# Optimization experiments

Measured on AMD Instinct MI355X. Metric: run time of the kernel, lower is better.

## Reference

```python
import jax, jax.numpy as jnp
import numpy as np

DIM = 1024
HEADS = 16
HEAD_DIM = DIM // HEADS
B, N = 2, 2048
SCALE = 1.0 / np.float32(np.sqrt(DIM))  # original scales by sqrt(dim), not sqrt(head_dim)


def setup_inputs() -> dict:
    key = jax.random.key(0)
    ks = jax.random.split(key, 9)
    s = 0.02
    return {
        "x": jax.random.normal(ks[0], (B, N, DIM), dtype=jnp.float32),
        "Wq": jax.random.normal(ks[1], (DIM, DIM), dtype=jnp.float32) * s,
        "bq": jax.random.normal(ks[2], (DIM,), dtype=jnp.float32) * s,
        "Wk": jax.random.normal(ks[3], (DIM, DIM), dtype=jnp.float32) * s,
        "bk": jax.random.normal(ks[4], (DIM,), dtype=jnp.float32) * s,
        "Wv": jax.random.normal(ks[5], (DIM, DIM), dtype=jnp.float32) * s,
        "bv": jax.random.normal(ks[6], (DIM,), dtype=jnp.float32) * s,
        "Wo": jax.random.normal(ks[7], (DIM, DIM), dtype=jnp.float32) * s,
        "bo": jax.random.normal(ks[8], (DIM,), dtype=jnp.float32) * s,
    }


def _split_heads(t):
    # torch.stack(torch.split(t, head_dim, -1), dim=0) -> (H, B, N, head_dim)
    b, n, _ = t.shape
    return jnp.moveaxis(t.reshape(b, n, HEADS, HEAD_DIM), 2, 0)


def reference(x, Wq, bq, Wk, bk, Wv, bv, Wo, bo):
    q = _split_heads(x @ Wq.T + bq)  # (H,B,N,d)
    k = _split_heads(x @ Wk.T + bk)
    v = _split_heads(x @ Wv.T + bv)
    # NOTE: original computes K @ Q^T (K rows attend over Q rows), scaled by sqrt(dim)
    scores = jnp.einsum("hbnd,hbmd->hbnm", k, q) * SCALE  # (H,B,N,N)
    attn = jax.nn.softmax(scores, axis=-1)
    out = jnp.einsum("hbnm,hbmd->hbnd", attn, v)  # (H,B,N,d)
    out = jnp.moveaxis(out, 0, 2).reshape(x.shape[0], x.shape[1], DIM)  # (B,N,H*d)
    return out @ Wo.T + bo
```

## Files before the change

kernel.cpp:

```cpp
#include <hip/hip_runtime.h>
#include <hip/hip_bf16.h>
#include <cstdint>
#include <cstddef>

typedef __bf16 bf16_t;
typedef __bf16 bf16x4 __attribute__((ext_vector_type(4)));
typedef __bf16 bf16x8 __attribute__((ext_vector_type(8)));
typedef float  f32x4  __attribute__((ext_vector_type(4)));
typedef float  f32x16 __attribute__((ext_vector_type(16)));
typedef unsigned int u32;
typedef unsigned int u32x4 __attribute__((ext_vector_type(4)));

#define DIM_   1024
#define HEADS_ 16
#define HD_    64
#define BB_    2
#define NN_    2048
#define MTOT   (BB_*NN_)
static constexpr float SCALE_ = 0.03125f;
static constexpr float EXPC_  = 0.045084220027780106f;

__device__ __forceinline__ float exp2_hw(float x) {
    float r;
    asm("v_exp_f32 %0, %1" : "=v"(r) : "v"(x));
    return r;
}

__global__ __launch_bounds__(256) void cvt_all(
    const float* __restrict__ X,
    const float* __restrict__ W0, const float* __restrict__ W1,
    const float* __restrict__ W2, const float* __restrict__ W3,
    bf16_t* __restrict__ xo,
    bf16_t* __restrict__ o0, bf16_t* __restrict__ o1,
    bf16_t* __restrict__ o2, bf16_t* __restrict__ o3)
{
    const int bid = blockIdx.x;
    const float* src;
    bf16_t* dst;
    int lb;
    if (bid < 2048) { src = X; dst = xo; lb = bid; }
    else {
        const int w = (bid - 2048) >> 9;
        lb = (bid - 2048) & 511;
        src = (w == 0) ? W0 : (w == 1) ? W1 : (w == 2) ? W2 : W3;
        dst = (w == 0) ? o0 : (w == 1) ? o1 : (w == 2) ? o2 : o3;
    }
    const size_t i = ((size_t)lb * 256 + threadIdx.x) * 8;
    f32x4 a = *(const f32x4*)(src + i);
    f32x4 b = *(const f32x4*)(src + i + 4);
    bf16x8 o;
    o[0] = (bf16_t)a.x; o[1] = (bf16_t)a.y; o[2] = (bf16_t)a.z; o[3] = (bf16_t)a.w;
    o[4] = (bf16_t)b.x; o[5] = (bf16_t)b.y; o[6] = (bf16_t)b.z; o[7] = (bf16_t)b.w;
    *(bf16x8*)(dst + i) = o;
}

__device__ __forceinline__ void gld16(const bf16_t* g, bf16_t* l) {
    __builtin_amdgcn_global_load_lds(
        (const __attribute__((address_space(1))) unsigned int*)g,
        (__attribute__((address_space(3))) unsigned int*)l, 16, 0, 0);
}

__global__ __launch_bounds__(512) void gemm_qkv(
    const bf16_t* __restrict__ A,
    const bf16_t* __restrict__ Wq, const bf16_t* __restrict__ Wk, const bf16_t* __restrict__ Wv,
    const float* __restrict__ bq, const float* __restrict__ bk, const float* __restrict__ bv,
    bf16_t* __restrict__ Cq, bf16_t* __restrict__ Ck, bf16_t* __restrict__ Cv)
{
    __shared__ __align__(16) bf16_t As[128 * 64];
    __shared__ __align__(16) bf16_t Bs[3][64 * 64];

    const int tid  = threadIdx.x;
    const int lane = tid & 63;
    const int w    = tid >> 6;
    const int wr   = w >> 1;
    const int wc   = w & 1;
    const int bn   = blockIdx.x;
    const int bm   = blockIdx.y;

    const int l15 = lane & 15;
    const int g   = lane >> 4;

    const int srow = lane >> 3;
    const int scol = (lane & 7) * 8;

    f32x4 aq[2][2], ak[2][2], av[2][2];
    #pragma unroll
    for (int i = 0; i < 2; i++)
        #pragma unroll
        for (int j = 0; j < 2; j++) {
            aq[i][j] = (f32x4){0.f, 0.f, 0.f, 0.f};
            ak[i][j] = (f32x4){0.f, 0.f, 0.f, 0.f};
            av[i][j] = (f32x4){0.f, 0.f, 0.f, 0.f};
        }

    for (int kb = 0; kb < DIM_; kb += 64) {
        __syncthreads();
        #pragma unroll
        for (int c2 = 0; c2 < 2; c2++) {
            const int chunk = w * 2 + c2;
            gld16(A + (size_t)(bm * 128 + chunk * 8 + srow) * DIM_ + kb + scol,
                  As + chunk * 512);
        }
        gld16(Wq + (size_t)(bn * 64 + w * 8 + srow) * DIM_ + kb + scol, &Bs[0][0] + w * 512);
        gld16(Wk + (size_t)(bn * 64 + w * 8 + srow) * DIM_ + kb + scol, &Bs[1][0] + w * 512);
        gld16(Wv + (size_t)(bn * 64 + w * 8 + srow) * DIM_ + kb + scol, &Bs[2][0] + w * 512);
        __syncthreads();

        #pragma unroll
        for (int kk = 0; kk < 2; kk++) {
            bf16x8 af[2];
            #pragma unroll
            for (int i = 0; i < 2; i++)
                af[i] = *(const bf16x8*)&As[(wr * 32 + i * 16 + l15) * 64 + kk * 32 + g * 8];
            bf16x8 bqf[2], bkf[2], bvf[2];
            #pragma unroll
            for (int j = 0; j < 2; j++) {
                const int off = (wc * 32 + j * 16 + l15) * 64 + kk * 32 + g * 8;
                bqf[j] = *(const bf16x8*)&Bs[0][off];
                bkf[j] = *(const bf16x8*)&Bs[1][off];
                bvf[j] = *(const bf16x8*)&Bs[2][off];
            }
            #pragma unroll
            for (int i = 0; i < 2; i++)
                #pragma unroll
                for (int j = 0; j < 2; j++) {
                    aq[i][j] = __builtin_amdgcn_mfma_f32_16x16x32_bf16(af[i], bqf[j], aq[i][j], 0, 0, 0);
                    ak[i][j] = __builtin_amdgcn_mfma_f32_16x16x32_bf16(af[i], bkf[j], ak[i][j], 0, 0, 0);
                    av[i][j] = __builtin_amdgcn_mfma_f32_16x16x32_bf16(af[i], bvf[j], av[i][j], 0, 0, 0);
                }
        }
    }

    const int r4 = g * 4;
    #pragma unroll
    for (int j = 0; j < 2; j++) {
        const int gc = bn * 64 + wc * 32 + j * 16 + l15;
        const float vq = bq[gc], vk = bk[gc], vv = bv[gc];
        #pragma unroll
        for (int i = 0; i < 2; i++) {
            #pragma unroll
            for (int r = 0; r < 4; r++) {
                const size_t gr = (size_t)(bm * 128 + wr * 32 + i * 16 + r4 + r) * DIM_ + gc;
                Cq[gr] = (bf16_t)((aq[i][j][r] + vq) * EXPC_);
                Ck[gr] = (bf16_t)(ak[i][j][r] + vk);
                Cv[gr] = (bf16_t)(av[i][j][r] + vv);
            }
        }
    }
}

__global__ __launch_bounds__(512) void gemm_o(
    const bf16_t* __restrict__ A, const bf16_t* __restrict__ Wo,
    const float* __restrict__ bo, float* __restrict__ C)
{
    __shared__ __align__(16) bf16_t As[64 * 64];
    __shared__ __align__(16) bf16_t Bs[128 * 64];

    const int tid  = threadIdx.x;
    const int lane = tid & 63;
    const int w    = tid >> 6;
    const int wr   = w & 1;
    const int wc   = w >> 1;
    const int bn   = blockIdx.x;
    const int bm   = blockIdx.y;

    const int l15 = lane & 15;
    const int g   = lane >> 4;

    const int srow = lane >> 3;
    const int scol = (lane & 7) * 8;

    f32x4 acc[2][2];
    #pragma unroll
    for (int i = 0; i < 2; i++)
        #pragma unroll
        for (int j = 0; j < 2; j++)
            acc[i][j] = (f32x4){0.f, 0.f, 0.f, 0.f};

    for (int kb = 0; kb < DIM_; kb += 64) {
        __syncthreads();
        gld16(A + (size_t)(bm * 64 + w * 8 + srow) * DIM_ + kb + scol, As + w * 512);
        #pragma unroll
        for (int c2 = 0; c2 < 2; c2++) {
            const int chunk = w * 2 + c2;
            gld16(Wo + (size_t)(bn * 128 + chunk * 8 + srow) * DIM_ + kb + scol,
                  Bs + chunk * 512);
        }
        __syncthreads();

        #pragma unroll
        for (int kk = 0; kk < 2; kk++) {
            bf16x8 af[2], bf[2];
            #pragma unroll
            for (int i = 0; i < 2; i++)
                af[i] = *(const bf16x8*)&As[(wr * 32 + i * 16 + l15) * 64 + kk * 32 + g * 8];
            #pragma unroll
            for (int j = 0; j < 2; j++)
                bf[j] = *(const bf16x8*)&Bs[(wc * 32 + j * 16 + l15) * 64 + kk * 32 + g * 8];
            #pragma unroll
            for (int i = 0; i < 2; i++)
                #pragma unroll
                for (int j = 0; j < 2; j++)
                    acc[i][j] = __builtin_amdgcn_mfma_f32_16x16x32_bf16(af[i], bf[j], acc[i][j], 0, 0, 0);
        }
    }

    const int r4 = g * 4;
    #pragma unroll
    for (int j = 0; j < 2; j++) {
        const int gc = bn * 128 + wc * 32 + j * 16 + l15;
        const float bv = bo[gc];
        #pragma unroll
        for (int i = 0; i < 2; i++) {
            #pragma unroll
            for (int r = 0; r < 4; r++) {
                const size_t gr = (size_t)(bm * 64 + wr * 32 + i * 16 + r4 + r) * DIM_ + gc;
                C[gr] = acc[i][j][r] + bv;
            }
        }
    }
}

__global__ __launch_bounds__(256) void transpose_v(
    const bf16_t* __restrict__ V, bf16_t* __restrict__ Vt)
{
    __shared__ __align__(16) bf16_t Ts[64 * 72];
    const int tid = threadIdx.x;
    const int mt  = blockIdx.x;
    const int bh  = blockIdx.y;
    const int b   = bh >> 4, h = bh & 15;
    const int m0  = mt * 64;
    const int r   = tid >> 2;
    const int c   = (tid & 3) * 16;

    const bf16x8* s = (const bf16x8*)(V + ((size_t)(b * NN_ + m0 + r)) * DIM_ + h * HD_ + c);
    *(bf16x8*)(Ts + r * 72 + c)     = s[0];
    *(bf16x8*)(Ts + r * 72 + c + 8) = s[1];
    __syncthreads();

    bf16x8 o0, o1;
    #pragma unroll
    for (int i = 0; i < 8; i++) o0[i] = Ts[(c + i) * 72 + r];
    #pragma unroll
    for (int i = 0; i < 8; i++) o1[i] = Ts[(c + 8 + i) * 72 + r];
    bf16_t* dst = Vt + ((size_t)bh * HD_ + r) * NN_ + m0 + c;
    *(bf16x8*)dst       = o0;
    *(bf16x8*)(dst + 8) = o1;
}

__device__ __forceinline__ u32 cvtpk_bf16(float lo, float hi) {
    u32 d;
    asm volatile("v_cvt_pk_bf16_f32 %0, %1, %2" : "=v"(d) : "v"(lo), "v"(hi));
    return d;
}

__global__ __launch_bounds__(512, 4) void attn_mfma7(
    const bf16_t* __restrict__ Qa,
    const bf16_t* __restrict__ Ka,
    const bf16_t* __restrict__ Vtg,
    bf16_t* __restrict__ O)
{
    __shared__ __align__(16) bf16_t Kt[2][128 * 72];
    __shared__ __align__(16) bf16_t Vt[2][64 * 136];

    const int tid  = threadIdx.x;
    const int lane = tid & 63;
    const int w    = tid >> 6;
    const int l31  = lane & 31;
    const int h5   = lane >> 5;

    const int nw = (w & 3) * 32;
    const int mo = (w >> 2) * 64;

    const int wg = blockIdx.x;
    const int id = (wg & 7) * 64 + (wg >> 3);
    const int bh = id >> 4;
    const int nt = id & 15;
    const int b  = bh >> 4, h = bh & 15;
    const int n0 = nt * 128;

    const size_t base = (size_t)b * NN_ * DIM_ + h * HD_;

    const bf16_t* qrow = Qa + base + (size_t)(n0 + nw + l31) * DIM_ + h5 * 8;
    bf16x8 qf[4];
    #pragma unroll
    for (int ks = 0; ks < 4; ks++)
        qf[ks] = *(const bf16x8*)(qrow + ks * 16);

    u32x4 onesw;
    onesw.x = 0x3F803F80u; onesw.y = 0x3F803F80u; onesw.z = 0x3F803F80u; onesw.w = 0x3F803F80u;
    const bf16x8 onesf = __builtin_bit_cast(bf16x8, onesw);

    f32x16 oa0 = {}, oa1 = {}, oL = {};

    const bf16_t* vrow   = Vtg + (size_t)bh * HD_ * NN_;
    const bf16_t* kgbase = Ka + base;

    const int kr2 = tid >> 3;
    const int kc2 = (tid & 7) * 8;
    const int vc2 = (tid & 7) * 16;

    bf16x8 kA0, kB0, vA0, vA1;

    #define ISSUE(m0)                                                                        \
        {                                                                                    \
            kA0 = *(const bf16x8*)(kgbase + (size_t)((m0) + kr2) * DIM_ + kc2);              \
            kB0 = *(const bf16x8*)(kgbase + (size_t)((m0) + 64 + kr2) * DIM_ + kc2);         \
            const bf16x8* vp = (const bf16x8*)(vrow + (size_t)kr2 * NN_ + (m0) + vc2);       \
            vA0 = vp[0]; vA1 = vp[1];                                                        \
        }
    #define COMMIT(buf)                                                                      \
        {                                                                                    \
            *(bf16x8*)(Kt[buf] + kr2 * 72 + kc2)        = kA0;                               \
            *(bf16x8*)(Kt[buf] + (64 + kr2) * 72 + kc2) = kB0;                               \
            bf16_t* vd = Vt[buf] + kr2 * 136 + vc2;                                          \
            *(bf16x8*)(vd)     = vA0;                                                        \
            *(bf16x8*)(vd + 8) = vA1;                                                        \
        }

    ISSUE(0);
    COMMIT(0);
    __syncthreads();

    for (int mt = 0; mt < NN_ / 128; mt++) {
        const int cur = mt & 1;
        if (mt < NN_ / 128 - 1) ISSUE((mt + 1) * 128);

        const bf16_t* KtC = Kt[cur];
        const bf16_t* VtC = Vt[cur];

        f32x16 sa0 = {}, sa1 = {};
        __builtin_amdgcn_s_setprio(1);
        #pragma unroll
        for (int ks = 0; ks < 4; ks++) {
            bf16x8 kf0 = *(const bf16x8*)&KtC[(mo + l31) * 72 + ks * 16 + h5 * 8];
            bf16x8 kf1 = *(const bf16x8*)&KtC[(mo + 32 + l31) * 72 + ks * 16 + h5 * 8];
            sa0 = __builtin_amdgcn_mfma_f32_32x32x16_bf16(kf0, qf[ks], sa0, 0, 0, 0);
            sa1 = __builtin_amdgcn_mfma_f32_32x32x16_bf16(kf1, qf[ks], sa1, 0, 0, 0);
        }
        __builtin_amdgcn_s_setprio(0);

        float p0[16], p1[16];
        #pragma unroll
        for (int r = 0; r < 16; r++) { p0[r] = exp2_hw(sa0[r]); p1[r] = exp2_hw(sa1[r]); }

        bf16x8 pf[4];
        #pragma unroll
        for (int mb = 0; mb < 4; mb++) {
            const float* pp = (mb & 2) ? p1 : p0;
            const int rb = (mb & 1) * 8;
            u32 x0 = cvtpk_bf16(pp[rb + 0], pp[rb + 1]);
            u32 x1 = cvtpk_bf16(pp[rb + 2], pp[rb + 3]);
            u32 y0 = cvtpk_bf16(pp[rb + 4], pp[rb + 5]);
            u32 y1 = cvtpk_bf16(pp[rb + 6], pp[rb + 7]);
            asm volatile("v_permlane32_swap_b32 %0, %1" : "+v"(x0), "+v"(y0));
            asm volatile("v_permlane32_swap_b32 %0, %1" : "+v"(x1), "+v"(y1));
            u32x4 t; t.x = x0; t.y = x1; t.z = y0; t.w = y1;
            pf[mb] = __builtin_bit_cast(bf16x8, t);
        }

        __builtin_amdgcn_s_setprio(1);
        #pragma unroll
        for (int ms = 0; ms < 4; ms++) {
            bf16x8 vf0 = *(const bf16x8*)&VtC[l31 * 136 + mo + ms * 16 + h5 * 8];
            bf16x8 vf1 = *(const bf16x8*)&VtC[(32 + l31) * 136 + mo + ms * 16 + h5 * 8];
            oa0 = __builtin_amdgcn_mfma_f32_32x32x16_bf16(pf[ms], vf0, oa0, 0, 0, 0);
            oa1 = __builtin_amdgcn_mfma_f32_32x32x16_bf16(pf[ms], vf1, oa1, 0, 0, 0);
            oL  = __builtin_amdgcn_mfma_f32_32x32x16_bf16(pf[ms], onesf, oL, 0, 0, 0);
        }
        __builtin_amdgcn_s_setprio(0);

        if (mt < NN_ / 128 - 1) COMMIT(cur ^ 1);
        __syncthreads();
    }
    #undef ISSUE
    #undef COMMIT

    if (w >= 4) {
        float* buf = (w < 6) ? ((float*)Kt + (w - 4) * 3072)
                             : ((float*)Vt + (w - 6) * 3072);
        #pragma unroll
        for (int reg = 0; reg < 16; reg++) {
            buf[reg * 64 + lane]        = oa0[reg];
            buf[1024 + reg * 64 + lane] = oa1[reg];
            buf[2048 + reg * 64 + lane] = oL[reg];
        }
    }
    __syncthreads();
    if (w < 4) {
        const float* buf = (w < 2) ? ((const float*)Kt + w * 3072)
                                   : ((const float*)Vt + (w - 2) * 3072);
        #pragma unroll
        for (int reg = 0; reg < 16; reg++) {
            oa0[reg] += buf[reg * 64 + lane];
            oa1[reg] += buf[1024 + reg * 64 + lane];
            oL[reg]  += buf[2048 + reg * 64 + lane];
        }
        #pragma unroll
        for (int reg = 0; reg < 16; reg++) {
            const int nr = (reg & 3) + 8 * (reg >> 2) + 4 * h5;
            const float il = 1.f / oL[reg];
            const size_t rowoff = base + (size_t)(n0 + nw + nr) * DIM_;
            O[rowoff + l31]      = (bf16_t)(oa0[reg] * il);
            O[rowoff + 32 + l31] = (bf16_t)(oa1[reg] * il);
        }
    }
}

extern "C" void kernel_launch(void* const* d_in, const int* in_sizes, int n_in,
                              void* d_out, int out_size, void* d_ws, size_t ws_size,
                              hipStream_t stream)
{
    const float* x  = (const float*)d_in[0];
    const float* Wq = (const float*)d_in[1];
    const float* bq = (const float*)d_in[2];
    const float* Wk = (const float*)d_in[3];
    const float* bk = (const float*)d_in[4];
    const float* Wv = (const float*)d_in[5];
    const float* bv = (const float*)d_in[6];
    const float* Wo = (const float*)d_in[7];
    const float* bo = (const float*)d_in[8];
    float* out = (float*)d_out;

    const size_t SEG = (size_t)MTOT * DIM_;
    bf16_t* xb = (bf16_t*)d_ws;
    bf16_t* qb = xb + SEG;
    bf16_t* kb = qb + SEG;
    bf16_t* vb = kb + SEG;
    bf16_t* vt = xb;
    bf16_t* ab = vb;

    bf16_t* wqb = vb + SEG;
    bf16_t* wkb = wqb + (size_t)DIM_ * DIM_;
    bf16_t* wvb = wkb + (size_t)DIM_ * DIM_;
    bf16_t* wob = wvb + (size_t)DIM_ * DIM_;

    cvt_all<<<dim3(4096), 256, 0, stream>>>(x, Wq, Wk, Wv, Wo, xb, wqb, wkb, wvb, wob);

    gemm_qkv<<<dim3(16, 32), 512, 0, stream>>>(
        xb, wqb, wkb, wvb, bq, bk, bv, qb, kb, vb);

    dim3 gt(NN_ / 64, BB_ * HEADS_);
    transpose_v<<<gt, 256, 0, stream>>>(vb, vt);

    attn_mfma7<<<dim3(512), 512, 0, stream>>>(kb, qb, vt, ab);

    gemm_o<<<dim3(8, 64), 512, 0, stream>>>(ab, wob, bo, out);
}
```

Baseline: 125.3 us.

## Double-buffer QKV/O GEMM LDS loads and compute softmax denominator with VALU sums

Both projection GEMMs now use two LDS buffers, so the next K tile is fetched with global_load_lds while the current one feeds the MFMAs, and each iteration needs one barrier instead of two. The QKV GEMM also moves to 32-wide K steps with a reworked per-wave load assignment. In attention, the extra MFMA against a ones vector that produced the row sum is replaced by per-lane VALU additions, a lane shuffle and a small LDS exchange. This frees MFMA issue slots and registers, but adds VALU work, an extra barrier and LDS traffic in the epilogue.

```diff
diff --git a/kernel.cpp b/kernel.cpp
--- a/kernel.cpp
+++ b/kernel.cpp
@@ -66,8 +66,8 @@
     const float* __restrict__ bq, const float* __restrict__ bk, const float* __restrict__ bv,
     bf16_t* __restrict__ Cq, bf16_t* __restrict__ Ck, bf16_t* __restrict__ Cv)
 {
-    __shared__ __align__(16) bf16_t As[128 * 64];
-    __shared__ __align__(16) bf16_t Bs[3][64 * 64];
+    __shared__ __align__(16) bf16_t As[2][128 * 32];
+    __shared__ __align__(16) bf16_t Bs[2][3 * 64 * 32];
 
     const int tid  = threadIdx.x;
     const int lane = tid & 63;
@@ -80,8 +80,15 @@
     const int l15 = lane & 15;
     const int g   = lane >> 4;
 
-    const int srow = lane >> 3;
-    const int scol = (lane & 7) * 8;
+    const int srow = lane >> 2;
+    const int scol = (lane & 3) * 8;
+
+    const bf16_t* aSrc  = A + (size_t)(bm * 128 + 16 * w + srow) * DIM_ + scol;
+    const bf16_t* w1p   = (w < 4) ? Wq : Wk;
+    const bf16_t* b1Src = w1p + (size_t)(bn * 64 + 16 * (w & 3) + srow) * DIM_ + scol;
+    const bf16_t* b2Src = Wv  + (size_t)(bn * 64 + 16 * w + srow) * DIM_ + scol;
+    const int b1Off = ((w < 4) ? 0 : 2048) + (w & 3) * 512;
+    const int b2Off = 4096 + w * 512;
 
     f32x4 aq[2][2], ak[2][2], av[2][2];
     #pragma unroll
@@ -93,43 +100,44 @@
             av[i][j] = (f32x4){0.f, 0.f, 0.f, 0.f};
         }
 
-    for (int kb = 0; kb < DIM_; kb += 64) {
+    #define QSTAGE(buf, kb)                                        \
+        {                                                          \
+            gld16(aSrc + (kb), &As[buf][w * 512]);                 \
+            gld16(b1Src + (kb), &Bs[buf][b1Off]);                  \
+            if (w < 4) gld16(b2Src + (kb), &Bs[buf][b2Off]);       \
+        }
+
+    QSTAGE(0, 0);
+    __syncthreads();
+
+    for (int t = 0; t < 32; t++) {
+        const int cur = t & 1;
+        if (t < 31) QSTAGE(cur ^ 1, (t + 1) * 32);
+
+        bf16x8 af[2];
+        #pragma unroll
+        for (int i = 0; i < 2; i++)
+            af[i] = *(const bf16x8*)&As[cur][(wr * 32 + i * 16 + l15) * 32 + g * 8];
+        bf16x8 bqf[2], bkf[2], bvf[2];
+        #pragma unroll
+        for (int j = 0; j < 2; j++) {
+            const int off = (wc * 32 + j * 16 + l15) * 32 + g * 8;
+            bqf[j] = *(const bf16x8*)&Bs[cur][off];
+            bkf[j] = *(const bf16x8*)&Bs[cur][2048 + off];
+            bvf[j] = *(const bf16x8*)&Bs[cur][4096 + off];
+        }
+        #pragma unroll
+        for (int i = 0; i < 2; i++)
+            #pragma unroll
+            for (int j = 0; j < 2; j++) {
+                aq[i][j] = __builtin_amdgcn_mfma_f32_16x16x32_bf16(af[i], bqf[j], aq[i][j], 0, 0, 0);
+                ak[i][j] = __builtin_amdgcn_mfma_f32_16x16x32_bf16(af[i], bkf[j], ak[i][j], 0, 0, 0);
+                av[i][j] = __builtin_amdgcn_mfma_f32_16x16x32_bf16(af[i], bvf[j], av[i][j], 0, 0, 0);
+            }
+
         __syncthreads();
-        #pragma unroll
-        for (int c2 = 0; c2 < 2; c2++) {
-            const int chunk = w * 2 + c2;
-            gld16(A + (size_t)(bm * 128 + chunk * 8 + srow) * DIM_ + kb + scol,
-                  As + chunk * 512);
-        }
-        gld16(Wq + (size_t)(bn * 64 + w * 8 + srow) * DIM_ + kb + scol, &Bs[0][0] + w * 512);
-        gld16(Wk + (size_t)(bn * 64 + w * 8 + srow) * DIM_ + kb + scol, &Bs[1][0] + w * 512);
-        gld16(Wv + (size_t)(bn * 64 + w * 8 + srow) * DIM_ + kb + scol, &Bs[2][0] + w * 512);
-        __syncthreads();
-
-        #pragma unroll
-        for (int kk = 0; kk < 2; kk++) {
-            bf16x8 af[2];
-            #pragma unroll
-            for (int i = 0; i < 2; i++)
-                af[i] = *(const bf16x8*)&As[(wr * 32 + i * 16 + l15) * 64 + kk * 32 + g * 8];
-            bf16x8 bqf[2], bkf[2], bvf[2];
-            #pragma unroll
-            for (int j = 0; j < 2; j++) {
-                const int off = (wc * 32 + j * 16 + l15) * 64 + kk * 32 + g * 8;
-                bqf[j] = *(const bf16x8*)&Bs[0][off];
-                bkf[j] = *(const bf16x8*)&Bs[1][off];
-                bvf[j] = *(const bf16x8*)&Bs[2][off];
-            }
-            #pragma unroll
-            for (int i = 0; i < 2; i++)
-                #pragma unroll
-                for (int j = 0; j < 2; j++) {
-                    aq[i][j] = __builtin_amdgcn_mfma_f32_16x16x32_bf16(af[i], bqf[j], aq[i][j], 0, 0, 0);
-                    ak[i][j] = __builtin_amdgcn_mfma_f32_16x16x32_bf16(af[i], bkf[j], ak[i][j], 0, 0, 0);
-                    av[i][j] = __builtin_amdgcn_mfma_f32_16x16x32_bf16(af[i], bvf[j], av[i][j], 0, 0, 0);
-                }
-        }
-    }
+    }
+    #undef QSTAGE
 
     const int r4 = g * 4;
     #pragma unroll
@@ -153,8 +161,8 @@
     const bf16_t* __restrict__ A, const bf16_t* __restrict__ Wo,
     const float* __restrict__ bo, float* __restrict__ C)
 {
-    __shared__ __align__(16) bf16_t As[64 * 64];
-    __shared__ __align__(16) bf16_t Bs[128 * 64];
+    __shared__ __align__(16) bf16_t As[2][64 * 64];
+    __shared__ __align__(16) bf16_t Bs[2][128 * 64];
 
     const int tid  = threadIdx.x;
     const int lane = tid & 63;
@@ -170,6 +178,10 @@
     const int srow = lane >> 3;
     const int scol = (lane & 7) * 8;
 
+    const bf16_t* aSrc  = A  + (size_t)(bm * 64 + w * 8 + srow) * DIM_ + scol;
+    const bf16_t* b0Src = Wo + (size_t)(bn * 128 + (w * 2 + 0) * 8 + srow) * DIM_ + scol;
+    const bf16_t* b1Src = Wo + (size_t)(bn * 128 + (w * 2 + 1) * 8 + srow) * DIM_ + scol;
+
     f32x4 acc[2][2];
     #pragma unroll
     for (int i = 0; i < 2; i++)
@@ -177,33 +189,39 @@
         for (int j = 0; j < 2; j++)
             acc[i][j] = (f32x4){0.f, 0.f, 0.f, 0.f};
 
-    for (int kb = 0; kb < DIM_; kb += 64) {
-        __syncthreads();
-        gld16(A + (size_t)(bm * 64 + w * 8 + srow) * DIM_ + kb + scol, As + w * 512);
-        #pragma unroll
-        for (int c2 = 0; c2 < 2; c2++) {
-            const int chunk = w * 2 + c2;
-            gld16(Wo + (size_t)(bn * 128 + chunk * 8 + srow) * DIM_ + kb + scol,
-                  Bs + chunk * 512);
-        }
-        __syncthreads();
+    #define OSTAGE(buf, kb)                                          \
+        {                                                            \
+            gld16(aSrc + (kb), &As[buf][w * 512]);                   \
+            gld16(b0Src + (kb), &Bs[buf][(w * 2 + 0) * 512]);        \
+            gld16(b1Src + (kb), &Bs[buf][(w * 2 + 1) * 512]);        \
+        }
+
+    OSTAGE(0, 0);
+    __syncthreads();
+
+    for (int t = 0; t < 16; t++) {
+        const int cur = t & 1;
+        if (t < 15) OSTAGE(cur ^ 1, (t + 1) * 64);
 
         #pragma unroll
         for (int kk = 0; kk < 2; kk++) {
             bf16x8 af[2], bf[2];
             #pragma unroll
             for (int i = 0; i < 2; i++)
-                af[i] = *(const bf16x8*)&As[(wr * 32 + i * 16 + l15) * 64 + kk * 32 + g * 8];
+                af[i] = *(const bf16x8*)&As[cur][(wr * 32 + i * 16 + l15) * 64 + kk * 32 + g * 8];
             #pragma unroll
             for (int j = 0; j < 2; j++)
-                bf[j] = *(const bf16x8*)&Bs[(wc * 32 + j * 16 + l15) * 64 + kk * 32 + g * 8];
+                bf[j] = *(const bf16x8*)&Bs[cur][(wc * 32 + j * 16 + l15) * 64 + kk * 32 + g * 8];
             #pragma unroll
             for (int i = 0; i < 2; i++)
                 #pragma unroll
                 for (int j = 0; j < 2; j++)
                     acc[i][j] = __builtin_amdgcn_mfma_f32_16x16x32_bf16(af[i], bf[j], acc[i][j], 0, 0, 0);
         }
-    }
+
+        __syncthreads();
+    }
+    #undef OSTAGE
 
     const int r4 = g * 4;
     #pragma unroll
@@ -254,7 +272,7 @@
     return d;
 }
 
-__global__ __launch_bounds__(512, 4) void attn_mfma7(
+__global__ __launch_bounds__(512, 4) void attn_mfma9(
     const bf16_t* __restrict__ Qa,
     const bf16_t* __restrict__ Ka,
     const bf16_t* __restrict__ Vtg,
@@ -287,11 +305,8 @@
     for (int ks = 0; ks < 4; ks++)
         qf[ks] = *(const bf16x8*)(qrow + ks * 16);
 
-    u32x4 onesw;
-    onesw.x = 0x3F803F80u; onesw.y = 0x3F803F80u; onesw.z = 0x3F803F80u; onesw.w = 0x3F803F80u;
-    const bf16x8 onesf = __builtin_bit_cast(bf16x8, onesw);
-
-    f32x16 oa0 = {}, oa1 = {}, oL = {};
+    f32x16 oa0 = {}, oa1 = {};
+    float Lp = 0.f;
 
     const bf16_t* vrow   = Vtg + (size_t)bh * HD_ * NN_;
     const bf16_t* kgbase = Ka + base;
@@ -343,6 +358,17 @@
         float p0[16], p1[16];
         #pragma unroll
         for (int r = 0; r < 16; r++) { p0[r] = exp2_hw(sa0[r]); p1[r] = exp2_hw(sa1[r]); }
+        {
+            float s0 = (p0[0] + p0[1]) + (p0[2] + p0[3]);
+            float s1 = (p0[4] + p0[5]) + (p0[6] + p0[7]);
+            float s2 = (p0[8] + p0[9]) + (p0[10] + p0[11]);
+            float s3 = (p0[12] + p0[13]) + (p0[14] + p0[15]);
+            float t0 = (p1[0] + p1[1]) + (p1[2] + p1[3]);
+            float t1 = (p1[4] + p1[5]) + (p1[6] + p1[7]);
+            float t2 = (p1[8] + p1[9]) + (p1[10] + p1[11]);
+            float t3 = (p1[12] + p1[13]) + (p1[14] + p1[15]);
+            Lp += ((s0 + s1) + (s2 + s3)) + ((t0 + t1) + (t2 + t3));
+        }
 
         bf16x8 pf[4];
         #pragma unroll
@@ -366,7 +392,6 @@
             bf16x8 vf1 = *(const bf16x8*)&VtC[(32 + l31) * 136 + mo + ms * 16 + h5 * 8];
             oa0 = __builtin_amdgcn_mfma_f32_32x32x16_bf16(pf[ms], vf0, oa0, 0, 0, 0);
             oa1 = __builtin_amdgcn_mfma_f32_32x32x16_bf16(pf[ms], vf1, oa1, 0, 0, 0);
-            oL  = __builtin_amdgcn_mfma_f32_32x32x16_bf16(pf[ms], onesf, oL, 0, 0, 0);
         }
         __builtin_amdgcn_s_setprio(0);
 
@@ -376,30 +401,42 @@
     #undef ISSUE
     #undef COMMIT
 
+    Lp += __shfl_xor(Lp, 32);
+
+    float* scratch0 = (float*)Kt;
+    float* scratch1 = (float*)Vt;
     if (w >= 4) {
-        float* buf = (w < 6) ? ((float*)Kt + (w - 4) * 3072)
-                             : ((float*)Vt + (w - 6) * 3072);
+        float* buf = (w < 6) ? (scratch0 + (w - 4) * 2112)
+                             : (scratch1 + (w - 6) * 2112);
         #pragma unroll
         for (int reg = 0; reg < 16; reg++) {
             buf[reg * 64 + lane]        = oa0[reg];
             buf[1024 + reg * 64 + lane] = oa1[reg];
-            buf[2048 + reg * 64 + lane] = oL[reg];
-        }
+        }
+        buf[2048 + lane] = Lp;
     }
     __syncthreads();
     if (w < 4) {
-        const float* buf = (w < 2) ? ((const float*)Kt + w * 3072)
-                                   : ((const float*)Vt + (w - 2) * 3072);
+        const float* buf = (w < 2) ? (scratch0 + w * 2112)
+                                   : (scratch1 + (w - 2) * 2112);
         #pragma unroll
         for (int reg = 0; reg < 16; reg++) {
             oa0[reg] += buf[reg * 64 + lane];
             oa1[reg] += buf[1024 + reg * 64 + lane];
-            oL[reg]  += buf[2048 + reg * 64 + lane];
-        }
+        }
+        Lp += buf[2048 + lane];
+    }
+    __syncthreads();
+
+    float* Lsh = scratch0 + 4224;
+    if (w < 4) Lsh[nw + l31] = Lp;
+    __syncthreads();
+
+    if (w < 4) {
         #pragma unroll
         for (int reg = 0; reg < 16; reg++) {
             const int nr = (reg & 3) + 8 * (reg >> 2) + 4 * h5;
-            const float il = 1.f / oL[reg];
+            const float il = 1.f / Lsh[nw + nr];
             const size_t rowoff = base + (size_t)(n0 + nw + nr) * DIM_;
             O[rowoff + l31]      = (bf16_t)(oa0[reg] * il);
             O[rowoff + 32 + l31] = (bf16_t)(oa1[reg] * il);
@@ -443,7 +480,7 @@
     dim3 gt(NN_ / 64, BB_ * HEADS_);
     transpose_v<<<gt, 256, 0, stream>>>(vb, vt);
 
-    attn_mfma7<<<dim3(512), 512, 0, stream>>>(kb, qb, vt, ab);
+    attn_mfma9<<<dim3(512), 512, 0, stream>>>(kb, qb, vt, ab);
 
     gemm_o<<<dim3(8, 64), 512, 0, stream>>>(ab, wob, bo, out);
 }
```

Result: faster. 118.1 us (-5.7%).
